# Optimization experiments

Measured on AMD Instinct MI355X. Metric: run time of the kernel, lower is better.

Reference implementation:

```python
import jax, jax.numpy as jnp
import numpy as np

B, T, C = 4, 2048, 1024


def wkv(k, v, w, u, reverse):
    """RWKV WKV scan with running-max stabilization.
    k, v: [B, T, C]; w, u: [C]. Returns y: [B, T, C]."""
    def step(carry, kv):
        num, den, mx = carry          # each [B, C]
        k_t, v_t = kv                 # each [B, C]
        ku = k_t + u
        m = jnp.maximum(mx, ku)
        e1 = jnp.exp(mx - m)
        e2 = jnp.exp(ku - m)
        y = (e1 * num + e2 * v_t) / (e1 * den + e2)
        # state update with decay w
        mw = mx + w
        mn = jnp.maximum(mw, k_t)
        e1s = jnp.exp(mw - mn)
        e2s = jnp.exp(k_t - mn)
        return (e1s * num + e2s * v_t, e1s * den + e2s, mn), y

    z = jnp.zeros_like(k[:, 0])
    init = (z, z, jnp.full_like(z, -1e38))
    ks = jnp.swapaxes(k, 0, 1)  # [T, B, C]
    vs = jnp.swapaxes(v, 0, 1)
    _, ys = jax.lax.scan(step, init, (ks, vs), reverse=reverse)
    return jnp.swapaxes(ys, 0, 1)


def setup_inputs() -> dict:
    key = jax.random.key(0)
    k1, k2, k3, k4, k5, k6, k7 = jax.random.split(key, 7)
    x = jax.random.normal(k1, (B, T, C), dtype=jnp.float32)
    rkv_w = jax.random.normal(k2, (6 * C, C), dtype=jnp.float32) / np.sqrt(C)
    out_w = jax.random.normal(k3, (C, 2 * C), dtype=jnp.float32) / np.sqrt(2 * C)
    time_decay = jax.random.uniform(k4, (C,), jnp.float32, -6.0, -5.0)
    time_first = jax.random.uniform(k5, (C,), jnp.float32, -3.0, 0.0)
    time_decay_rev = jax.random.uniform(k6, (C,), jnp.float32, -6.0, -5.0)
    time_first_rev = jax.random.uniform(k7, (C,), jnp.float32, -3.0, 0.0)
    return {"x": x, "rkv_w": rkv_w, "out_w": out_w,
            "time_decay": time_decay, "time_first": time_first,
            "time_decay_rev": time_decay_rev, "time_first_rev": time_first_rev}


def reference(x, rkv_w, out_w, time_decay, time_first, time_decay_rev, time_first_rev):
    b, t, c = x.shape
    rkv = jnp.einsum('btc,dc->btd', x, rkv_w).reshape(b, t, 2, 3, c)
    r_f, k_f, v_f = rkv[:, :, 0, 0], rkv[:, :, 0, 1], rkv[:, :, 0, 2]
    r_b, k_b, v_b = rkv[:, :, 1, 0], rkv[:, :, 1, 1], rkv[:, :, 1, 2]
    out_f = jax.nn.sigmoid(r_f) * wkv(k_f, v_f, -jnp.exp(time_decay), time_first, False)
    out_b = jax.nn.sigmoid(r_b) * wkv(k_b, v_b, -jnp.exp(time_decay_rev), time_first_rev, True)
    out_cat = jnp.concatenate([out_f, out_b], axis=-1)  # [B, T, 2C]
    return jnp.einsum('btd,cd->btc', out_cat, out_w)
```

## Files before the change

### kernel.cpp

```cpp
#include <hip/hip_runtime.h>
#include <cstdint>
#include <cstddef>

#define Bdim 4
#define Tdim 2048
#define Cdim 1024

#define SEG  32
#define CHB  32
#define LSEG (Tdim / SEG)

#define G1_K   1024
#define G1_N   6144
#define G1_NKT 32
#define G1_GXT 48
#define G1_NWG 1536

typedef __attribute__((ext_vector_type(8))) short bf16x8;
typedef __attribute__((ext_vector_type(4))) float f32x4;

__device__ __forceinline__ unsigned short f2bf(float f) {
    unsigned int u = __float_as_uint(f);
    u += 0x7fffu + ((u >> 16) & 1u);
    return (unsigned short)(u >> 16);
}
__device__ __forceinline__ float bf2f(unsigned short h) {
    return __uint_as_float((unsigned int)h << 16);
}

__device__ __forceinline__ void gload_lds16(const void* g, void* l) {
    __builtin_amdgcn_global_load_lds(
        (const __attribute__((address_space(1))) unsigned int*)g,
        (__attribute__((address_space(3))) unsigned int*)l,
        16, 0, 0);
}

__global__ __launch_bounds__(256) void cast_all(
    const float* __restrict__ x,  unsigned short* __restrict__ xb,  int n1,
    const float* __restrict__ w1, unsigned short* __restrict__ wb,  int n2,
    const float* __restrict__ w2, unsigned short* __restrict__ ob,  int n3)
{
    int i = blockIdx.x * 256 + threadIdx.x;
    const float* in; unsigned short* out;
    if (i < n1)           { in = x;  out = xb; }
    else if (i < n1 + n2) { in = w1; out = wb; i -= n1; }
    else if (i < n1 + n2 + n3) { in = w2; out = ob; i -= n1 + n2; }
    else return;
    float4 v = ((const float4*)in)[i];
    ushort4 o;
    o.x = f2bf(v.x); o.y = f2bf(v.y); o.z = f2bf(v.z); o.w = f2bf(v.w);
    ((ushort4*)out)[i] = o;
}

__device__ __forceinline__ void stage_128(
    const unsigned short* __restrict__ G, int row0, int K, int elemoff,
    char* slot, int wave, int lane)
{
    const int sl = (lane & 3) ^ ((lane >> 3) & 3);
    const unsigned short* gp = G + (size_t)(row0 + wave * 16 + (lane >> 2)) * K
                                 + elemoff + sl * 8;
    gload_lds16(gp, slot + wave * 1024);
}

__global__ __launch_bounds__(512, 4) void gemm1_3slot(
    const unsigned short* __restrict__ A, const unsigned short* __restrict__ B,
    unsigned short* __restrict__ C)
{
    __shared__ char ldsb[73728];

    const int tid  = threadIdx.x;
    const int wave = tid >> 6;
    const int lane = tid & 63;
    const int wm = wave >> 1;
    const int wn = wave & 1;
    const int fr = lane & 15;
    const int cswz = (((lane >> 4) ^ ((fr >> 1) & 3)) << 4);

    const int swz = (blockIdx.x & 7) * (G1_NWG >> 3) + (blockIdx.x >> 3);
    const int bx  = swz % G1_GXT;
    const int by  = swz / G1_GXT;
    const int m0 = by * 256;
    const int n0 = bx * 128;

    f32x4 acc[4][4] = {};

    stage_128(A, m0,       G1_K, 0,  ldsb + 0,            wave, lane);
    stage_128(A, m0 + 128, G1_K, 0,  ldsb + 8192,         wave, lane);
    stage_128(B, n0,       G1_K, 0,  ldsb + 49152,        wave, lane);
    stage_128(A, m0,       G1_K, 32, ldsb + 16384,        wave, lane);
    stage_128(A, m0 + 128, G1_K, 32, ldsb + 16384 + 8192, wave, lane);
    stage_128(B, n0,       G1_K, 32, ldsb + 49152 + 8192, wave, lane);
    asm volatile("s_waitcnt vmcnt(3)" ::: "memory");
    __builtin_amdgcn_s_barrier();
    __builtin_amdgcn_sched_barrier(0);

    int sR = 0;
    for (int t = 0; t < G1_NKT; ++t) {
        const int sW = (sR >= 1) ? sR - 1 : 2;
        int kst = t + 2; if (kst > G1_NKT - 1) kst = G1_NKT - 1;
        const int keoff = kst * 32;

        const char* Asl = ldsb + sR * 16384;
        const char* Bsl = ldsb + 49152 + sR * 8192;

        bf16x8 af[4], bq[4];
        #pragma unroll
        for (int i_ = 0; i_ < 4; ++i_)
            af[i_] = *(const bf16x8*)(Asl + (wm * 64 + i_ * 16 + fr) * 64 + cswz);
        #pragma unroll
        for (int j_ = 0; j_ < 4; ++j_)
            bq[j_] = *(const bf16x8*)(Bsl + (wn * 64 + j_ * 16 + fr) * 64 + cswz);

        stage_128(A, m0,       G1_K, keoff, ldsb + sW * 16384,        wave, lane);
        stage_128(A, m0 + 128, G1_K, keoff, ldsb + sW * 16384 + 8192, wave, lane);
        stage_128(B, n0,       G1_K, keoff, ldsb + 49152 + sW * 8192, wave, lane);

        __builtin_amdgcn_s_barrier();
        __builtin_amdgcn_sched_barrier(0);
        __builtin_amdgcn_s_setprio(1);
        #pragma unroll
        for (int i_ = 0; i_ < 4; ++i_)
            #pragma unroll
            for (int j_ = 0; j_ < 4; ++j_)
                acc[i_][j_] = __builtin_amdgcn_mfma_f32_16x16x32_bf16(
                    af[i_], bq[j_], acc[i_][j_], 0, 0, 0);
        __builtin_amdgcn_s_setprio(0);
        asm volatile("s_waitcnt vmcnt(3)" ::: "memory");
        __builtin_amdgcn_s_barrier();
        __builtin_amdgcn_sched_barrier(0);

        sR = (sR < 2) ? sR + 1 : 0;
    }

    #pragma unroll
    for (int i_ = 0; i_ < 4; ++i_) {
        const int row = m0 + wm * 64 + i_ * 16 + (lane >> 4) * 4;
        #pragma unroll
        for (int j_ = 0; j_ < 4; ++j_) {
            const int col = n0 + wn * 64 + j_ * 16 + fr;
            #pragma unroll
            for (int r = 0; r < 4; ++r)
                C[(size_t)(row + r) * G1_N + col] = f2bf(acc[i_][j_][r]);
        }
    }
}

__global__ __launch_bounds__(256) void gemm_bf16_nt(
    const unsigned short* __restrict__ A, const unsigned short* __restrict__ B,
    float* __restrict__ C, int M, int N, int K)
{
    __shared__ unsigned short As[128 * 32];
    __shared__ unsigned short Bs[128 * 32];

    const int tid  = threadIdx.x;
    const int wave = tid >> 6;
    const int lane = tid & 63;
    const int m0 = blockIdx.y * 128;
    const int n0 = blockIdx.x * 128;
    const int wr = wave >> 1, wc = wave & 1;

    const int srow = tid >> 2;
    const int scol = (tid & 3) * 8;
    const unsigned short* Ag = A + (size_t)(m0 + srow) * K + scol;
    const unsigned short* Bg = B + (size_t)(n0 + srow) * K + scol;
    char* AsW = (char*)As + wave * 1024;
    char* BsW = (char*)Bs + wave * 1024;

    f32x4 acc[4][4] = {};

    const int fr = lane & 15;
    const int fk = (lane >> 4) * 8;

    for (int k0 = 0; k0 < K; k0 += 32) {
        gload_lds16(Ag + k0,                  AsW);
        gload_lds16(Ag + k0 + (size_t)64 * K, AsW + 4096);
        gload_lds16(Bg + k0,                  BsW);
        gload_lds16(Bg + k0 + (size_t)64 * K, BsW + 4096);
        __syncthreads();

        bf16x8 af[4], bfr_[4];
        #pragma unroll
        for (int f = 0; f < 4; ++f) {
            af[f]   = *(const bf16x8*)&As[(wr * 64 + f * 16 + fr) * 32 + fk];
            bfr_[f] = *(const bf16x8*)&Bs[(wc * 64 + f * 16 + fr) * 32 + fk];
        }
        #pragma unroll
        for (int i = 0; i < 4; ++i)
            #pragma unroll
            for (int j = 0; j < 4; ++j)
                acc[i][j] = __builtin_amdgcn_mfma_f32_16x16x32_bf16(
                    af[i], bfr_[j], acc[i][j], 0, 0, 0);
        __syncthreads();
    }

    #pragma unroll
    for (int i = 0; i < 4; ++i) {
        const int row = m0 + wr * 64 + i * 16 + (lane >> 4) * 4;
        #pragma unroll
        for (int j = 0; j < 4; ++j) {
            const int col = n0 + wc * 64 + j * 16 + (lane & 15);
            #pragma unroll
            for (int r = 0; r < 4; ++r)
                C[(size_t)(row + r) * N + col] = acc[i][j][r];
        }
    }
}

__global__ __launch_bounds__(1024) void wkv_scan_par(
    const unsigned short* __restrict__ rkv,
    const float* __restrict__ td,  const float* __restrict__ tf,
    const float* __restrict__ tdr, const float* __restrict__ tfr,
    unsigned short* __restrict__ outcat)
{
    __shared__ float sBn[SEG][CHB], sBd[SEG][CHB], sMb[SEG][CHB];

    const int tid = threadIdx.x;
    const int ch  = tid & (CHB - 1);
    const int seg = tid >> 5;

    const int bi  = blockIdx.x;
    const int b   = bi >> 6;
    const int rem = bi & 63;
    const int dir = rem >> 5;
    const int c   = (rem & 31) * CHB + ch;

    const float w = -__expf(dir ? tdr[c] : td[c]);
    const float u = dir ? tfr[c] : tf[c];

    const int strideT = 6 * Cdim;
    const int tstep   = dir ? -strideT : strideT;
    const int t0      = dir ? (Tdim - 1 - seg * LSEG) : (seg * LSEG);

    const unsigned short* pbase = rkv + ((size_t)b * Tdim + t0) * strideT + dir * 3 * Cdim + c;

    const int PF = 8;

    float bn = 0.0f, bd = 0.0f, mb = -1e38f;
    {
        const unsigned short* q = pbase;
        float kk[PF], vv[PF];
        #pragma unroll
        for (int i = 0; i < PF; ++i) {
            kk[i] = bf2f(q[Cdim]); vv[i] = bf2f(q[2 * Cdim]); q += tstep;
        }
        for (int t = 0; t < LSEG; t += PF) {
            float kn[PF], vn[PF];
            if (t + PF < LSEG) {
                #pragma unroll
                for (int i = 0; i < PF; ++i) {
                    kn[i] = bf2f(q[Cdim]); vn[i] = bf2f(q[2 * Cdim]); q += tstep;
                }
            }
            #pragma unroll
            for (int i = 0; i < PF; ++i) {
                const float k_ = kk[i], v_ = vv[i];
                const float mw = mb + w;
                const float mn = fmaxf(mw, k_);
                const float e1 = __expf(mw - mn);
                const float e2 = __expf(k_ - mn);
                bn = e1 * bn + e2 * v_;
                bd = e1 * bd + e2;
                mb = mn;
            }
            #pragma unroll
            for (int i = 0; i < PF; ++i) { kk[i] = kn[i]; vv[i] = vn[i]; }
        }
    }
    sBn[seg][ch] = bn; sBd[seg][ch] = bd; sMb[seg][ch] = mb;
    __syncthreads();

    if (tid < CHB) {
        float n = 0.0f, d = 0.0f, m = -1e38f;
        const float a = w * (float)LSEG;
        for (int s = 0; s < SEG; ++s) {
            const float tn = sBn[s][tid], tdn = sBd[s][tid], tm = sMb[s][tid];
            sBn[s][tid] = n; sBd[s][tid] = d; sMb[s][tid] = m;
            const float ma = m + a;
            const float mm = fmaxf(ma, tm);
            const float e1 = __expf(ma - mm);
            const float e2 = __expf(tm - mm);
            n = e1 * n + e2 * tn;
            d = e1 * d + e2 * tdn;
            m = mm;
        }
    }
    __syncthreads();

    float num = sBn[seg][ch], den = sBd[seg][ch], mx = sMb[seg][ch];
    {
        const unsigned short* q = pbase;
        unsigned short* po = outcat + ((size_t)b * Tdim + t0) * (2 * Cdim) + dir * Cdim + c;
        const int ostep = dir ? -(2 * Cdim) : (2 * Cdim);

        float rr[PF], kk[PF], vv[PF];
        #pragma unroll
        for (int i = 0; i < PF; ++i) {
            rr[i] = bf2f(q[0]); kk[i] = bf2f(q[Cdim]); vv[i] = bf2f(q[2 * Cdim]); q += tstep;
        }
        for (int t = 0; t < LSEG; t += PF) {
            float rn[PF], kn[PF], vn[PF];
            if (t + PF < LSEG) {
                #pragma unroll
                for (int i = 0; i < PF; ++i) {
                    rn[i] = bf2f(q[0]); kn[i] = bf2f(q[Cdim]); vn[i] = bf2f(q[2 * Cdim]); q += tstep;
                }
            }
            #pragma unroll
            for (int i = 0; i < PF; ++i) {
                const float k_ = kk[i], v_ = vv[i], r_ = rr[i];
                const float ku = k_ + u;
                const float m  = fmaxf(mx, ku);
                const float e1 = __expf(mx - m);
                const float e2 = __expf(ku - m);
                const float y  = (e1 * num + e2 * v_) / (e1 * den + e2);
                const float sr = 1.0f / (1.0f + __expf(-r_));
                *po = f2bf(sr * y);
                po += ostep;
                const float mw  = mx + w;
                const float mn  = fmaxf(mw, k_);
                const float e1s = __expf(mw - mn);
                const float e2s = __expf(k_ - mn);
                num = e1s * num + e2s * v_;
                den = e1s * den + e2s;
                mx  = mn;
            }
            #pragma unroll
            for (int i = 0; i < PF; ++i) { rr[i] = rn[i]; kk[i] = kn[i]; vv[i] = vn[i]; }
        }
    }
}

extern "C" void kernel_launch(void* const* d_in, const int* in_sizes, int n_in,
                              void* d_out, int out_size, void* d_ws, size_t ws_size,
                              hipStream_t stream)
{
    const float* x    = (const float*)d_in[0];
    const float* rkvw = (const float*)d_in[1];
    const float* outw = (const float*)d_in[2];
    const float* td   = (const float*)d_in[3];
    const float* tf   = (const float*)d_in[4];
    const float* tdr  = (const float*)d_in[5];
    const float* tfr  = (const float*)d_in[6];
    float* out = (float*)d_out;

    const int M = Bdim * Tdim;

    char* ws = (char*)d_ws;
    unsigned short* rkv = (unsigned short*)ws;
    unsigned short* xb  = (unsigned short*)(ws + 100663296);
    unsigned short* wb  = (unsigned short*)(ws + 117440512);
    unsigned short* ob  = (unsigned short*)(ws + 130023424);
    unsigned short* cat = (unsigned short*)(ws + 134217728);

    const int n1 = M * Cdim / 4;
    const int n2 = 6 * Cdim * Cdim / 4;
    const int n3 = Cdim * 2 * Cdim / 4;

    hipLaunchKernelGGL(cast_all, dim3((n1 + n2 + n3 + 255) / 256), dim3(256), 0, stream,
                       x, xb, n1, rkvw, wb, n2, outw, ob, n3);

    hipLaunchKernelGGL(gemm1_3slot, dim3(G1_NWG), dim3(512), 0, stream, xb, wb, rkv);

    hipLaunchKernelGGL(wkv_scan_par, dim3(Bdim * 2 * (Cdim / CHB)), dim3(1024), 0, stream,
                       rkv, td, tf, tdr, tfr, cat);

    hipLaunchKernelGGL(gemm_bf16_nt, dim3(Cdim / 128, M / 128), dim3(256), 0, stream,
                       cat, ob, out, M, Cdim, 2 * Cdim);
}
```

Baseline: 259.9 us.

## Process two channels per thread in WKV scan and remap GEMM1 tiles per XCD

The WKV scan now gives each thread two adjacent channels, loading and storing packed 32-bit bf16 pairs instead of 16-bit scalars. This halves the grid to 128 blocks of 1024 threads and doubles the independent dependency chains per thread. The aim is fewer, wider memory transactions and more instruction-level parallelism in the serial recurrence, at the cost of fewer blocks to occupy the GPU's compute units. Separately, the GEMM1 block-to-tile mapping is changed so each XCD owns a contiguous band of four M-row tiles, aiming for better L2 reuse of the A operand.

```diff
diff --git a/kernel.cpp b/kernel.cpp
--- a/kernel.cpp
+++ b/kernel.cpp
@@ -7,13 +7,11 @@
 #define Cdim 1024
 
 #define SEG  32
-#define CHB  32
 #define LSEG (Tdim / SEG)
 
 #define G1_K   1024
 #define G1_N   6144
 #define G1_NKT 32
-#define G1_GXT 48
 #define G1_NWG 1536
 
 typedef __attribute__((ext_vector_type(8))) short bf16x8;
@@ -26,6 +24,12 @@
 }
 __device__ __forceinline__ float bf2f(unsigned short h) {
     return __uint_as_float((unsigned int)h << 16);
+}
+__device__ __forceinline__ float bf2f_lo(unsigned int u) {
+    return __uint_as_float(u << 16);
+}
+__device__ __forceinline__ float bf2f_hi(unsigned int u) {
+    return __uint_as_float(u & 0xffff0000u);
 }
 
 __device__ __forceinline__ void gload_lds16(const void* g, void* l) {
@@ -76,9 +80,10 @@
     const int fr = lane & 15;
     const int cswz = (((lane >> 4) ^ ((fr >> 1) & 3)) << 4);
 
-    const int swz = (blockIdx.x & 7) * (G1_NWG >> 3) + (blockIdx.x >> 3);
-    const int bx  = swz % G1_GXT;
-    const int by  = swz / G1_GXT;
+    const int xcd = blockIdx.x & 7;
+    const int li  = blockIdx.x >> 3;
+    const int bx  = li >> 2;
+    const int by  = xcd * 4 + (li & 3);
     const int m0 = by * 256;
     const int n0 = bx * 128;
 
@@ -212,66 +217,88 @@
     const float* __restrict__ tdr, const float* __restrict__ tfr,
     unsigned short* __restrict__ outcat)
 {
-    __shared__ float sBn[SEG][CHB], sBd[SEG][CHB], sMb[SEG][CHB];
+    __shared__ float sBn[SEG][64], sBd[SEG][64], sMb[SEG][64];
 
     const int tid = threadIdx.x;
-    const int ch  = tid & (CHB - 1);
+    const int chg = tid & 31;
     const int seg = tid >> 5;
 
     const int bi  = blockIdx.x;
-    const int b   = bi >> 6;
-    const int rem = bi & 63;
-    const int dir = rem >> 5;
-    const int c   = (rem & 31) * CHB + ch;
-
-    const float w = -__expf(dir ? tdr[c] : td[c]);
-    const float u = dir ? tfr[c] : tf[c];
+    const int b   = bi >> 5;
+    const int rem = bi & 31;
+    const int dir = rem >> 4;
+    const int cbase = (rem & 15) * 64;
+    const int c0  = cbase + chg * 2;
+
+    const float w0 = -__expf(dir ? tdr[c0]     : td[c0]);
+    const float w1 = -__expf(dir ? tdr[c0 + 1] : td[c0 + 1]);
+    const float u0 = dir ? tfr[c0]     : tf[c0];
+    const float u1 = dir ? tfr[c0 + 1] : tf[c0 + 1];
 
     const int strideT = 6 * Cdim;
     const int tstep   = dir ? -strideT : strideT;
     const int t0      = dir ? (Tdim - 1 - seg * LSEG) : (seg * LSEG);
 
-    const unsigned short* pbase = rkv + ((size_t)b * Tdim + t0) * strideT + dir * 3 * Cdim + c;
+    const unsigned short* pbase = rkv + ((size_t)b * Tdim + t0) * strideT + dir * 3 * Cdim + c0;
 
     const int PF = 8;
 
-    float bn = 0.0f, bd = 0.0f, mb = -1e38f;
+    float bn0 = 0.f, bd0 = 0.f, mb0 = -1e38f;
+    float bn1 = 0.f, bd1 = 0.f, mb1 = -1e38f;
     {
         const unsigned short* q = pbase;
-        float kk[PF], vv[PF];
+        unsigned int kk[PF], vv[PF];
         #pragma unroll
         for (int i = 0; i < PF; ++i) {
-            kk[i] = bf2f(q[Cdim]); vv[i] = bf2f(q[2 * Cdim]); q += tstep;
+            kk[i] = *(const unsigned int*)(q + Cdim);
+            vv[i] = *(const unsigned int*)(q + 2 * Cdim);
+            q += tstep;
         }
         for (int t = 0; t < LSEG; t += PF) {
-            float kn[PF], vn[PF];
+            unsigned int kn[PF], vn[PF];
             if (t + PF < LSEG) {
                 #pragma unroll
                 for (int i = 0; i < PF; ++i) {
-                    kn[i] = bf2f(q[Cdim]); vn[i] = bf2f(q[2 * Cdim]); q += tstep;
+                    kn[i] = *(const unsigned int*)(q + Cdim);
+                    vn[i] = *(const unsigned int*)(q + 2 * Cdim);
+                    q += tstep;
                 }
             }
             #pragma unroll
             for (int i = 0; i < PF; ++i) {
-                const float k_ = kk[i], v_ = vv[i];
-                const float mw = mb + w;
-                const float mn = fmaxf(mw, k_);
-                const float e1 = __expf(mw - mn);
-                const float e2 = __expf(k_ - mn);
-                bn = e1 * bn + e2 * v_;
-                bd = e1 * bd + e2;
-                mb = mn;
+                {
+                    const float k_ = bf2f_lo(kk[i]), v_ = bf2f_lo(vv[i]);
+                    const float mw = mb0 + w0;
+                    const float mn = fmaxf(mw, k_);
+                    const float e1 = __expf(mw - mn);
+                    const float e2 = __expf(k_ - mn);
+                    bn0 = e1 * bn0 + e2 * v_;
+                    bd0 = e1 * bd0 + e2;
+                    mb0 = mn;
+                }
+                {
+                    const float k_ = bf2f_hi(kk[i]), v_ = bf2f_hi(vv[i]);
+                    const float mw = mb1 + w1;
+                    const float mn = fmaxf(mw, k_);
+                    const float e1 = __expf(mw - mn);
+                    const float e2 = __expf(k_ - mn);
+                    bn1 = e1 * bn1 + e2 * v_;
+                    bd1 = e1 * bd1 + e2;
+                    mb1 = mn;
+                }
             }
             #pragma unroll
             for (int i = 0; i < PF; ++i) { kk[i] = kn[i]; vv[i] = vn[i]; }
         }
     }
-    sBn[seg][ch] = bn; sBd[seg][ch] = bd; sMb[seg][ch] = mb;
+    sBn[seg][chg * 2] = bn0; sBd[seg][chg * 2] = bd0; sMb[seg][chg * 2] = mb0;
+    sBn[seg][chg * 2 + 1] = bn1; sBd[seg][chg * 2 + 1] = bd1; sMb[seg][chg * 2 + 1] = mb1;
     __syncthreads();
 
-    if (tid < CHB) {
-        float n = 0.0f, d = 0.0f, m = -1e38f;
-        const float a = w * (float)LSEG;
+    if (tid < 64) {
+        const float wv = -__expf(dir ? tdr[cbase + tid] : td[cbase + tid]);
+        const float a  = wv * (float)LSEG;
+        float n = 0.f, d = 0.f, m = -1e38f;
         for (int s = 0; s < SEG; ++s) {
             const float tn = sBn[s][tid], tdn = sBd[s][tid], tm = sMb[s][tid];
             sBn[s][tid] = n; sBd[s][tid] = d; sMb[s][tid] = m;
@@ -286,43 +313,71 @@
     }
     __syncthreads();
 
-    float num = sBn[seg][ch], den = sBd[seg][ch], mx = sMb[seg][ch];
+    float num0 = sBn[seg][chg * 2],     den0 = sBd[seg][chg * 2],     mx0 = sMb[seg][chg * 2];
+    float num1 = sBn[seg][chg * 2 + 1], den1 = sBd[seg][chg * 2 + 1], mx1 = sMb[seg][chg * 2 + 1];
     {
         const unsigned short* q = pbase;
-        unsigned short* po = outcat + ((size_t)b * Tdim + t0) * (2 * Cdim) + dir * Cdim + c;
+        unsigned short* po = outcat + ((size_t)b * Tdim + t0) * (2 * Cdim) + dir * Cdim + c0;
         const int ostep = dir ? -(2 * Cdim) : (2 * Cdim);
 
-        float rr[PF], kk[PF], vv[PF];
+        unsigned int rr[PF], kk[PF], vv[PF];
         #pragma unroll
         for (int i = 0; i < PF; ++i) {
-            rr[i] = bf2f(q[0]); kk[i] = bf2f(q[Cdim]); vv[i] = bf2f(q[2 * Cdim]); q += tstep;
+            rr[i] = *(const unsigned int*)(q);
+            kk[i] = *(const unsigned int*)(q + Cdim);
+            vv[i] = *(const unsigned int*)(q + 2 * Cdim);
+            q += tstep;
         }
         for (int t = 0; t < LSEG; t += PF) {
-            float rn[PF], kn[PF], vn[PF];
+            unsigned int rn[PF], kn[PF], vn[PF];
             if (t + PF < LSEG) {
                 #pragma unroll
                 for (int i = 0; i < PF; ++i) {
-                    rn[i] = bf2f(q[0]); kn[i] = bf2f(q[Cdim]); vn[i] = bf2f(q[2 * Cdim]); q += tstep;
+                    rn[i] = *(const unsigned int*)(q);
+                    kn[i] = *(const unsigned int*)(q + Cdim);
+                    vn[i] = *(const unsigned int*)(q + 2 * Cdim);
+                    q += tstep;
                 }
             }
             #pragma unroll
             for (int i = 0; i < PF; ++i) {
-                const float k_ = kk[i], v_ = vv[i], r_ = rr[i];
-                const float ku = k_ + u;
-                const float m  = fmaxf(mx, ku);
-                const float e1 = __expf(mx - m);
-                const float e2 = __expf(ku - m);
-                const float y  = (e1 * num + e2 * v_) / (e1 * den + e2);
-                const float sr = 1.0f / (1.0f + __expf(-r_));
-                *po = f2bf(sr * y);
+                unsigned int ow;
+                {
+                    const float k_ = bf2f_lo(kk[i]), v_ = bf2f_lo(vv[i]), r_ = bf2f_lo(rr[i]);
+                    const float ku = k_ + u0;
+                    const float m  = fmaxf(mx0, ku);
+                    const float e1 = __expf(mx0 - m);
+                    const float e2 = __expf(ku - m);
+                    const float y  = (e1 * num0 + e2 * v_) / (e1 * den0 + e2);
+                    const float sr = 1.0f / (1.0f + __expf(-r_));
+                    ow = (unsigned int)f2bf(sr * y);
+                    const float mw  = mx0 + w0;
+                    const float mn  = fmaxf(mw, k_);
+                    const float e1s = __expf(mw - mn);
+                    const float e2s = __expf(k_ - mn);
+                    num0 = e1s * num0 + e2s * v_;
+                    den0 = e1s * den0 + e2s;
+                    mx0  = mn;
+                }
+                {
+                    const float k_ = bf2f_hi(kk[i]), v_ = bf2f_hi(vv[i]), r_ = bf2f_hi(rr[i]);
+                    const float ku = k_ + u1;
+                    const float m  = fmaxf(mx1, ku);
+                    const float e1 = __expf(mx1 - m);
+                    const float e2 = __expf(ku - m);
+                    const float y  = (e1 * num1 + e2 * v_) / (e1 * den1 + e2);
+                    const float sr = 1.0f / (1.0f + __expf(-r_));
+                    ow |= ((unsigned int)f2bf(sr * y)) << 16;
+                    const float mw  = mx1 + w1;
+                    const float mn  = fmaxf(mw, k_);
+                    const float e1s = __expf(mw - mn);
+                    const float e2s = __expf(k_ - mn);
+                    num1 = e1s * num1 + e2s * v_;
+                    den1 = e1s * den1 + e2s;
+                    mx1  = mn;
+                }
+                *(unsigned int*)po = ow;
                 po += ostep;
-                const float mw  = mx + w;
-                const float mn  = fmaxf(mw, k_);
-                const float e1s = __expf(mw - mn);
-                const float e2s = __expf(k_ - mn);
-                num = e1s * num + e2s * v_;
-                den = e1s * den + e2s;
-                mx  = mn;
             }
             #pragma unroll
             for (int i = 0; i < PF; ++i) { rr[i] = rn[i]; kk[i] = kn[i]; vv[i] = vn[i]; }
@@ -361,7 +416,7 @@
 
     hipLaunchKernelGGL(gemm1_3slot, dim3(G1_NWG), dim3(512), 0, stream, xb, wb, rkv);
 
-    hipLaunchKernelGGL(wkv_scan_par, dim3(Bdim * 2 * (Cdim / CHB)), dim3(1024), 0, stream,
+    hipLaunchKernelGGL(wkv_scan_par, dim3(Bdim * 2 * 16), dim3(1024), 0, stream,
                        rkv, td, tf, tdr, tfr, cat);
 
     hipLaunchKernelGGL(gemm_bf16_nt, dim3(Cdim / 128, M / 128), dim3(256), 0, stream,
```

Result: slower. 265.9 us (+2.3%).

## Vectorize WKV scan to 4 channels per thread with finer segments

Applied to the files above, without the earlier changes.

Each scan thread now handles 4 adjacent channels, loading and storing them as 8-byte ushort4 words instead of scalar bf16. The time axis is split into 128 segments of 16 steps, which shortens each thread's serial chain, but the serial combine pass over segments grows fourfold. Division and sigmoid now use the hardware reciprocal approximation, at a small cost in accuracy. GEMM1 block swizzling is also remapped so each XCD handles a contiguous band of M tiles, to improve L2 reuse.

```diff
diff --git a/kernel.cpp b/kernel.cpp
--- a/kernel.cpp
+++ b/kernel.cpp
@@ -6,14 +6,12 @@
 #define Tdim 2048
 #define Cdim 1024
 
-#define SEG  32
-#define CHB  32
+#define SEG  128
 #define LSEG (Tdim / SEG)
 
 #define G1_K   1024
 #define G1_N   6144
 #define G1_NKT 32
-#define G1_GXT 48
 #define G1_NWG 1536
 
 typedef __attribute__((ext_vector_type(8))) short bf16x8;
@@ -24,8 +22,11 @@
     u += 0x7fffu + ((u >> 16) & 1u);
     return (unsigned short)(u >> 16);
 }
-__device__ __forceinline__ float bf2f(unsigned short h) {
+__device__ __forceinline__ float bfu(unsigned short h) {
     return __uint_as_float((unsigned int)h << 16);
+}
+__device__ __forceinline__ float frcp(float x) {
+    return __builtin_amdgcn_rcpf(x);
 }
 
 __device__ __forceinline__ void gload_lds16(const void* g, void* l) {
@@ -76,9 +77,10 @@
     const int fr = lane & 15;
     const int cswz = (((lane >> 4) ^ ((fr >> 1) & 3)) << 4);
 
-    const int swz = (blockIdx.x & 7) * (G1_NWG >> 3) + (blockIdx.x >> 3);
-    const int bx  = swz % G1_GXT;
-    const int by  = swz / G1_GXT;
+    const int xcd = blockIdx.x & 7;
+    const int li  = blockIdx.x >> 3;
+    const int bx  = li >> 2;
+    const int by  = xcd * 4 + (li & 3);
     const int m0 = by * 256;
     const int n0 = bx * 128;
 
@@ -212,66 +214,87 @@
     const float* __restrict__ tdr, const float* __restrict__ tfr,
     unsigned short* __restrict__ outcat)
 {
-    __shared__ float sBn[SEG][CHB], sBd[SEG][CHB], sMb[SEG][CHB];
+    __shared__ float sBn[SEG][32], sBd[SEG][32], sMb[SEG][32];
 
     const int tid = threadIdx.x;
-    const int ch  = tid & (CHB - 1);
-    const int seg = tid >> 5;
+    const int chg = tid & 7;
+    const int seg = tid >> 3;
 
     const int bi  = blockIdx.x;
     const int b   = bi >> 6;
     const int rem = bi & 63;
     const int dir = rem >> 5;
-    const int c   = (rem & 31) * CHB + ch;
-
-    const float w = -__expf(dir ? tdr[c] : td[c]);
-    const float u = dir ? tfr[c] : tf[c];
+    const int cbase = (rem & 31) * 32;
+    const int c0  = cbase + chg * 4;
+
+    float w[4], u[4];
+    #pragma unroll
+    for (int ch = 0; ch < 4; ++ch) {
+        w[ch] = -__expf(dir ? tdr[c0 + ch] : td[c0 + ch]);
+        u[ch] = dir ? tfr[c0 + ch] : tf[c0 + ch];
+    }
 
     const int strideT = 6 * Cdim;
     const int tstep   = dir ? -strideT : strideT;
     const int t0      = dir ? (Tdim - 1 - seg * LSEG) : (seg * LSEG);
 
-    const unsigned short* pbase = rkv + ((size_t)b * Tdim + t0) * strideT + dir * 3 * Cdim + c;
+    const unsigned short* pbase = rkv + ((size_t)b * Tdim + t0) * strideT + dir * 3 * Cdim + c0;
 
     const int PF = 8;
 
-    float bn = 0.0f, bd = 0.0f, mb = -1e38f;
+    float bn[4] = {0.f, 0.f, 0.f, 0.f};
+    float bd[4] = {0.f, 0.f, 0.f, 0.f};
+    float mb[4] = {-1e38f, -1e38f, -1e38f, -1e38f};
     {
         const unsigned short* q = pbase;
-        float kk[PF], vv[PF];
+        ushort4 kk[PF], vv[PF];
         #pragma unroll
         for (int i = 0; i < PF; ++i) {
-            kk[i] = bf2f(q[Cdim]); vv[i] = bf2f(q[2 * Cdim]); q += tstep;
+            kk[i] = *(const ushort4*)(q + Cdim);
+            vv[i] = *(const ushort4*)(q + 2 * Cdim);
+            q += tstep;
         }
         for (int t = 0; t < LSEG; t += PF) {
-            float kn[PF], vn[PF];
+            ushort4 kn[PF], vn[PF];
             if (t + PF < LSEG) {
                 #pragma unroll
                 for (int i = 0; i < PF; ++i) {
-                    kn[i] = bf2f(q[Cdim]); vn[i] = bf2f(q[2 * Cdim]); q += tstep;
+                    kn[i] = *(const ushort4*)(q + Cdim);
+                    vn[i] = *(const ushort4*)(q + 2 * Cdim);
+                    q += tstep;
                 }
             }
             #pragma unroll
             for (int i = 0; i < PF; ++i) {
-                const float k_ = kk[i], v_ = vv[i];
-                const float mw = mb + w;
-                const float mn = fmaxf(mw, k_);
-                const float e1 = __expf(mw - mn);
-                const float e2 = __expf(k_ - mn);
-                bn = e1 * bn + e2 * v_;
-                bd = e1 * bd + e2;
-                mb = mn;
+                const float kf[4] = {bfu(kk[i].x), bfu(kk[i].y), bfu(kk[i].z), bfu(kk[i].w)};
+                const float vf[4] = {bfu(vv[i].x), bfu(vv[i].y), bfu(vv[i].z), bfu(vv[i].w)};
+                #pragma unroll
+                for (int ch = 0; ch < 4; ++ch) {
+                    const float mw = mb[ch] + w[ch];
+                    const float mn = fmaxf(mw, kf[ch]);
+                    const float e1 = __expf(mw - mn);
+                    const float e2 = __expf(kf[ch] - mn);
+                    bn[ch] = e1 * bn[ch] + e2 * vf[ch];
+                    bd[ch] = e1 * bd[ch] + e2;
+                    mb[ch] = mn;
+                }
             }
             #pragma unroll
             for (int i = 0; i < PF; ++i) { kk[i] = kn[i]; vv[i] = vn[i]; }
         }
     }
-    sBn[seg][ch] = bn; sBd[seg][ch] = bd; sMb[seg][ch] = mb;
+    #pragma unroll
+    for (int ch = 0; ch < 4; ++ch) {
+        sBn[seg][chg * 4 + ch] = bn[ch];
+        sBd[seg][chg * 4 + ch] = bd[ch];
+        sMb[seg][chg * 4 + ch] = mb[ch];
+    }
     __syncthreads();
 
-    if (tid < CHB) {
-        float n = 0.0f, d = 0.0f, m = -1e38f;
-        const float a = w * (float)LSEG;
+    if (tid < 32) {
+        const float wv = -__expf(dir ? tdr[cbase + tid] : td[cbase + tid]);
+        const float a  = wv * (float)LSEG;
+        float n = 0.f, d = 0.f, m = -1e38f;
         for (int s = 0; s < SEG; ++s) {
             const float tn = sBn[s][tid], tdn = sBd[s][tid], tm = sMb[s][tid];
             sBn[s][tid] = n; sBd[s][tid] = d; sMb[s][tid] = m;
@@ -286,43 +309,64 @@
     }
     __syncthreads();
 
-    float num = sBn[seg][ch], den = sBd[seg][ch], mx = sMb[seg][ch];
+    float num[4], den[4], mx[4];
+    #pragma unroll
+    for (int ch = 0; ch < 4; ++ch) {
+        num[ch] = sBn[seg][chg * 4 + ch];
+        den[ch] = sBd[seg][chg * 4 + ch];
+        mx[ch]  = sMb[seg][chg * 4 + ch];
+    }
     {
         const unsigned short* q = pbase;
-        unsigned short* po = outcat + ((size_t)b * Tdim + t0) * (2 * Cdim) + dir * Cdim + c;
+        unsigned short* po = outcat + ((size_t)b * Tdim + t0) * (2 * Cdim) + dir * Cdim + c0;
         const int ostep = dir ? -(2 * Cdim) : (2 * Cdim);
 
-        float rr[PF], kk[PF], vv[PF];
+        ushort4 rr[PF], kk[PF], vv[PF];
         #pragma unroll
         for (int i = 0; i < PF; ++i) {
-            rr[i] = bf2f(q[0]); kk[i] = bf2f(q[Cdim]); vv[i] = bf2f(q[2 * Cdim]); q += tstep;
+            rr[i] = *(const ushort4*)(q);
+            kk[i] = *(const ushort4*)(q + Cdim);
+            vv[i] = *(const ushort4*)(q + 2 * Cdim);
+            q += tstep;
         }
         for (int t = 0; t < LSEG; t += PF) {
-            float rn[PF], kn[PF], vn[PF];
+            ushort4 rn[PF], kn[PF], vn[PF];
             if (t + PF < LSEG) {
                 #pragma unroll
                 for (int i = 0; i < PF; ++i) {
-                    rn[i] = bf2f(q[0]); kn[i] = bf2f(q[Cdim]); vn[i] = bf2f(q[2 * Cdim]); q += tstep;
+                    rn[i] = *(const ushort4*)(q);
+                    kn[i] = *(const ushort4*)(q + Cdim);
+                    vn[i] = *(const ushort4*)(q + 2 * Cdim);
+                    q += tstep;
                 }
             }
             #pragma unroll
             for (int i = 0; i < PF; ++i) {
-                const float k_ = kk[i], v_ = vv[i], r_ = rr[i];
-                const float ku = k_ + u;
-                const float m  = fmaxf(mx, ku);
-                const float e1 = __expf(mx - m);
-                const float e2 = __expf(ku - m);
-                const float y  = (e1 * num + e2 * v_) / (e1 * den + e2);
-                const float sr = 1.0f / (1.0f + __expf(-r_));
-                *po = f2bf(sr * y);
+                const float kf[4] = {bfu(kk[i].x), bfu(kk[i].y), bfu(kk[i].z), bfu(kk[i].w)};
+                const float vf[4] = {bfu(vv[i].x), bfu(vv[i].y), bfu(vv[i].z), bfu(vv[i].w)};
+                const float rf[4] = {bfu(rr[i].x), bfu(rr[i].y), bfu(rr[i].z), bfu(rr[i].w)};
+                unsigned short oy[4];
+                #pragma unroll
+                for (int ch = 0; ch < 4; ++ch) {
+                    const float ku = kf[ch] + u[ch];
+                    const float m  = fmaxf(mx[ch], ku);
+                    const float e1 = __expf(mx[ch] - m);
+                    const float e2 = __expf(ku - m);
+                    const float y  = (e1 * num[ch] + e2 * vf[ch]) * frcp(e1 * den[ch] + e2);
+                    const float sr = frcp(1.0f + __expf(-rf[ch]));
+                    oy[ch] = f2bf(sr * y);
+                    const float mw  = mx[ch] + w[ch];
+                    const float mn  = fmaxf(mw, kf[ch]);
+                    const float e1s = __expf(mw - mn);
+                    const float e2s = __expf(kf[ch] - mn);
+                    num[ch] = e1s * num[ch] + e2s * vf[ch];
+                    den[ch] = e1s * den[ch] + e2s;
+                    mx[ch]  = mn;
+                }
+                ushort4 ow;
+                ow.x = oy[0]; ow.y = oy[1]; ow.z = oy[2]; ow.w = oy[3];
+                *(ushort4*)po = ow;
                 po += ostep;
-                const float mw  = mx + w;
-                const float mn  = fmaxf(mw, k_);
-                const float e1s = __expf(mw - mn);
-                const float e2s = __expf(k_ - mn);
-                num = e1s * num + e2s * v_;
-                den = e1s * den + e2s;
-                mx  = mn;
             }
             #pragma unroll
             for (int i = 0; i < PF; ++i) { rr[i] = rn[i]; kk[i] = kn[i]; vv[i] = vn[i]; }
@@ -361,7 +405,7 @@
 
     hipLaunchKernelGGL(gemm1_3slot, dim3(G1_NWG), dim3(512), 0, stream, xb, wb, rkv);
 
-    hipLaunchKernelGGL(wkv_scan_par, dim3(Bdim * 2 * (Cdim / CHB)), dim3(1024), 0, stream,
+    hipLaunchKernelGGL(wkv_scan_par, dim3(Bdim * 2 * 32), dim3(1024), 0, stream,
                        rkv, td, tf, tdr, tfr, cat);
 
     hipLaunchKernelGGL(gemm_bf16_nt, dim3(Cdim / 128, M / 128), dim3(256), 0, stream,
```

After: 262.3 us. Within noise of the previous version (+0.9%).
